# Kernel optimization log

Hardware: AMD Instinct MI355X
Metric: run time of the kernel (lower is better)

The kernel has to match this reference:

```python
import jax, jax.numpy as jnp
import numpy as np

N_NODES = 100000
N_EDGES = 1600000
D = 64
N_TARGETS = 100
N_GRAPHS = 512


def gcn_conv(x, W, b, src, dst):
    """GCNConv with default add_self_loops=True, symmetric normalization."""
    n = x.shape[0]
    h = x @ W  # [N, out]
    ones = jnp.ones(dst.shape[0], dtype=h.dtype)
    deg = jax.ops.segment_sum(ones, dst, num_segments=n) + 1.0  # +1 for self-loop
    dinv = jax.lax.rsqrt(deg)
    norm = dinv[src] * dinv[dst]  # [E]
    agg = jax.ops.segment_sum(h[src] * norm[:, None], dst, num_segments=n)
    agg = agg + h * (dinv * dinv)[:, None]  # self-loop contribution: 1/deg[i] * h[i]
    return agg + b


def setup_inputs() -> dict:
    key = jax.random.key(0)
    ks = jax.random.split(key, 12)
    x = jax.random.normal(ks[0], (N_NODES, D), dtype=jnp.float32)
    edge_index = jax.random.randint(ks[1], (2, N_EDGES), 0, N_NODES, dtype=jnp.int64)
    batch_seg = jnp.sort(jax.random.randint(ks[2], (N_NODES,), 0, N_GRAPHS, dtype=jnp.int64))
    s = 1.0 / np.sqrt(D)
    W1 = jax.random.normal(ks[3], (D, D), dtype=jnp.float32) * s
    b1 = jnp.zeros((D,), dtype=jnp.float32)
    W2 = jax.random.normal(ks[4], (D, D), dtype=jnp.float32) * s
    b2 = jnp.zeros((D,), dtype=jnp.float32)
    W3 = jax.random.normal(ks[5], (D, D), dtype=jnp.float32) * s
    b3 = jnp.zeros((D,), dtype=jnp.float32)
    Wout = jax.random.normal(ks[6], (D, N_TARGETS), dtype=jnp.float32) * s
    bout = jnp.zeros((N_TARGETS,), dtype=jnp.float32)
    return {"x": x, "W1": W1, "b1": b1, "W2": W2, "b2": b2, "W3": W3, "b3": b3,
            "Wout": Wout, "bout": bout, "edge_index": edge_index, "batch_seg": batch_seg}


def reference(x, W1, b1, W2, b2, W3, b3, Wout, bout, edge_index, batch_seg):
    src, dst = edge_index[0], edge_index[1]
    h = jax.nn.relu(gcn_conv(x, W1, b1, src, dst))   # dropout p=0 -> identity
    h = jax.nn.relu(gcn_conv(h, W2, b2, src, dst))
    h = gcn_conv(h, W3, b3, src, dst)
    counts = jax.ops.segment_sum(jnp.ones(h.shape[0], h.dtype), batch_seg, num_segments=N_GRAPHS)
    pooled = jax.ops.segment_sum(h, batch_seg, num_segments=N_GRAPHS) / jnp.maximum(counts, 1.0)[:, None]
    return pooled @ Wout + bout  # [N_GRAPHS, N_TARGETS]
```

## Files before the change

### kernel.cpp

```cpp
#include <hip/hip_runtime.h>

#define N_NODES   100000
#define N_EDGES   1600000
#define D         64
#define N_TARGETS 100
#define N_GRAPHS  512
#define NBUCK     391
#define EPB       4096
#define BCAP      6144
#define MM_NPW    16

typedef _Float16 half4 __attribute__((ext_vector_type(4)));
typedef _Float16 half8 __attribute__((ext_vector_type(8)));
typedef __fp16   hf2   __attribute__((ext_vector_type(2)));
typedef __fp16   hf8   __attribute__((ext_vector_type(8)));

#if defined(__has_builtin)
#if __has_builtin(__builtin_amdgcn_fdot2)
#define USE_DOT2 1
#endif
#endif

__global__ void k_init(int* __restrict__ gcur, float* __restrict__ poolz) {
    int i = blockIdx.x * blockDim.x + threadIdx.x;
    if (i < NBUCK) gcur[i] = 0;
    if (i < N_GRAPHS * D + N_GRAPHS) poolz[i] = 0.0f;
}

__global__ void k_prepW(const float* __restrict__ W, _Float16* __restrict__ out) {
    int t = threadIdx.x;
#pragma unroll
    for (int it = 0; it < 2; ++it) {
        int idx = t + it * 256;
        int m = idx >> 3, c = idx & 7;
        half8 hv;
#pragma unroll
        for (int tt = 0; tt < 8; ++tt)
            hv[tt] = (_Float16)W[(8 * c + tt) * 64 + m];
        *(half8*)&out[m * 64 + ((c ^ (m & 7)) * 8)] = hv;
    }
}

__global__ void __launch_bounds__(256)
k_binA(const int* __restrict__ src, const int* __restrict__ dst,
       int* __restrict__ gcur, unsigned long long* __restrict__ staged) {
    __shared__ int hist[NBUCK];
    __shared__ int boff[NBUCK];
    int tid = threadIdx.x;
    for (int i = tid; i < NBUCK; i += 256) hist[i] = 0;
    __syncthreads();

    int e0 = blockIdx.x * EPB;
    int s_[16], d_[16], r_[16];
#pragma unroll
    for (int k = 0; k < 16; ++k) {
        int e = e0 + k * 256 + tid;
        if (e < N_EDGES) {
            s_[k] = src[e];
            d_[k] = dst[e];
            r_[k] = atomicAdd(&hist[d_[k] >> 8], 1);
        } else {
            d_[k] = -1;
        }
    }
    __syncthreads();
    for (int b = tid; b < NBUCK; b += 256) {
        int h = hist[b];
        boff[b] = (h > 0) ? atomicAdd(&gcur[b], h) : 0;
    }
    __syncthreads();
#pragma unroll
    for (int k = 0; k < 16; ++k) {
        if (d_[k] >= 0) {
            int b = d_[k] >> 8;
            staged[(size_t)b * BCAP + boff[b] + r_[k]] =
                ((unsigned long long)(unsigned)d_[k] << 32) | (unsigned)s_[k];
        }
    }
}

__global__ void k_scanB(const int* __restrict__ gcur, int* __restrict__ bstart) {
    __shared__ int s[512];
    int t = threadIdx.x;
    int v = (t < NBUCK) ? gcur[t] : 0;
    s[t] = v;
    __syncthreads();
    for (int off = 1; off < 512; off <<= 1) {
        int x = (t >= off) ? s[t - off] : 0;
        __syncthreads();
        s[t] += x;
        __syncthreads();
    }
    if (t < NBUCK) bstart[t] = s[t] - v;
    if (t == 0) bstart[NBUCK] = N_EDGES;
}

__global__ void __launch_bounds__(256)
k_binB(const unsigned long long* __restrict__ staged, const int* __restrict__ gcur,
       const int* __restrict__ bstart, int* __restrict__ esrc,
       int* __restrict__ base, float* __restrict__ dinv) {
    __shared__ int s[256];
    __shared__ int lbase[256];
    __shared__ int cur[256];
    int b = blockIdx.x;
    int t = threadIdx.x;
    int n0 = b << 8;
    int Eb = gcur[b];
    int Sb = bstart[b];
    const unsigned long long* sl = staged + (size_t)b * BCAP;

    cur[t] = 0;
    __syncthreads();
    for (int k = t; k < Eb; k += 256) {
        int dl = ((int)(sl[k] >> 32)) & 255;
        atomicAdd(&cur[dl], 1);
    }
    __syncthreads();
    int v = cur[t];
    s[t] = v;
    __syncthreads();
    for (int off = 1; off < 256; off <<= 1) {
        int x = (t >= off) ? s[t - off] : 0;
        __syncthreads();
        s[t] += x;
        __syncthreads();
    }
    lbase[t] = s[t] - v;
    int gi = n0 + t;
    if (gi < N_NODES) {
        base[gi] = Sb + (s[t] - v);
        dinv[gi] = rsqrtf((float)v + 1.0f);
    }
    if (b == 0 && t == 0) base[N_NODES] = N_EDGES;
    cur[t] = 0;
    __syncthreads();
    for (int k = t; k < Eb; k += 256) {
        unsigned long long pd = sl[k];
        int dl = ((int)(pd >> 32)) & 255;
        int pos = Sb + lbase[dl] + atomicAdd(&cur[dl], 1);
        esrc[pos] = (int)(pd & 0xffffffffu);
    }
}

__global__ void __launch_bounds__(256)
k_mm(const float* __restrict__ X, const float* __restrict__ W,
     const float* __restrict__ dinv, _Float16* __restrict__ Y16) {
    __shared__ float W1L[D * D];
    __shared__ float aSh[4][D];
    int tid = threadIdx.x;
#pragma unroll
    for (int it = 0; it < 4; ++it) {
        int idx = (tid + it * 256) * 4;
        *(float4*)&W1L[idx] = *(const float4*)(W + idx);
    }
    __syncthreads();

    int wv = tid >> 6, lane = tid & 63;
    float wreg[D];
#pragma unroll
    for (int k = 0; k < D; ++k)
        wreg[k] = W1L[k * D + lane];

    int i0 = (blockIdx.x * 4 + wv) * MM_NPW;
    if (i0 >= N_NODES) return;
    int iEnd = i0 + MM_NPW; if (iEnd > N_NODES) iEnd = N_NODES;

    float xv = X[(size_t)i0 * D + lane];
    for (int i = i0; i < iEnd; ++i) {
        int inext = (i + 1 < N_NODES) ? (i + 1) : i;
        float xnext = X[(size_t)inext * D + lane];

        aSh[wv][lane] = xv;
        asm volatile("s_waitcnt lgkmcnt(0)" ::: "memory");

        float ac0 = 0.f, ac1 = 0.f, ac2 = 0.f, ac3 = 0.f;
#pragma unroll
        for (int c = 0; c < 16; ++c) {
            float4 a4 = *(const float4*)&aSh[wv][c * 4];
            ac0 = fmaf(a4.x, wreg[4 * c + 0], ac0);
            ac1 = fmaf(a4.y, wreg[4 * c + 1], ac1);
            ac2 = fmaf(a4.z, wreg[4 * c + 2], ac2);
            ac3 = fmaf(a4.w, wreg[4 * c + 3], ac3);
        }
        float acc = (ac0 + ac1) + (ac2 + ac3);
        Y16[(size_t)i * D + lane] = (_Float16)(acc * dinv[i]);
        xv = xnext;
    }
}

__global__ void __launch_bounds__(256)
k_pullmm(const _Float16* __restrict__ H, const int* __restrict__ esrc,
         const int* __restrict__ base, const float* __restrict__ dinv,
         const float* __restrict__ b_in, const _Float16* __restrict__ Whg,
         _Float16* __restrict__ Hout) {
    __shared__ _Float16 WhL[D * D];
    __shared__ _Float16 aSh[4][D];
    {
#pragma unroll
        for (int it = 0; it < 2; ++it) {
            int t = threadIdx.x + it * 256;
            *(half8*)&WhL[t * 8] = *(const half8*)&Whg[t * 8];
        }
    }
    __syncthreads();

    int wv   = threadIdx.x >> 6;
    int lane = threadIdx.x & 63;
    int g = lane >> 3, l = lane & 7;
    int i    = blockIdx.x * 4 + wv;
    int s0 = base[i], s1 = base[i + 1];

    float acc[8] = {0.f, 0.f, 0.f, 0.f, 0.f, 0.f, 0.f, 0.f};
    if (g == 0) {
        half8 sv = *(const half8*)(H + (size_t)i * D + l * 8);
#pragma unroll
        for (int q = 0; q < 8; ++q) acc[q] = (float)sv[q];
    }

    int p = s0;
    while (p < s1) {
        int cnt = s1 - p;
        if (cnt > 64) cnt = 64;
        int ed = (lane < cnt) ? esrc[p + lane] : 0;
        int j = 0;
        for (; j + 32 <= cnt; j += 32) {
            int e0 = __shfl(ed, j + g, 64);
            int e1 = __shfl(ed, j + 8 + g, 64);
            int e2 = __shfl(ed, j + 16 + g, 64);
            int e3 = __shfl(ed, j + 24 + g, 64);
            half8 v0 = *(const half8*)(H + (size_t)(unsigned)e0 * D + l * 8);
            half8 v1 = *(const half8*)(H + (size_t)(unsigned)e1 * D + l * 8);
            half8 v2 = *(const half8*)(H + (size_t)(unsigned)e2 * D + l * 8);
            half8 v3 = *(const half8*)(H + (size_t)(unsigned)e3 * D + l * 8);
            half8 s01 = v0 + v1;
            half8 s23 = v2 + v3;
#pragma unroll
            for (int q = 0; q < 8; ++q)
                acc[q] += (float)s01[q] + (float)s23[q];
        }
        for (; j + 8 <= cnt; j += 8) {
            int e0 = __shfl(ed, j + g, 64);
            half8 v0 = *(const half8*)(H + (size_t)(unsigned)e0 * D + l * 8);
#pragma unroll
            for (int q = 0; q < 8; ++q) acc[q] += (float)v0[q];
        }
        if (j < cnt) {
            int idx = j + g;
            int e0 = __shfl(ed, idx & 63, 64);
            if (idx < cnt) {
                half8 v0 = *(const half8*)(H + (size_t)(unsigned)e0 * D + l * 8);
#pragma unroll
                for (int q = 0; q < 8; ++q) acc[q] += (float)v0[q];
            }
        }
        p += cnt;
    }
#pragma unroll
    for (int off = 8; off <= 32; off <<= 1) {
#pragma unroll
        for (int q = 0; q < 8; ++q)
            acc[q] += __shfl_xor(acc[q], off, 64);
    }

    float di = dinv[i];
    if (g == 0) {
        float4 bl0 = *(const float4*)(b_in + l * 8);
        float4 bl1 = *(const float4*)(b_in + l * 8 + 4);
        half8 av;
        av[0] = (_Float16)fmaxf(fmaf(acc[0], di, bl0.x), 0.f);
        av[1] = (_Float16)fmaxf(fmaf(acc[1], di, bl0.y), 0.f);
        av[2] = (_Float16)fmaxf(fmaf(acc[2], di, bl0.z), 0.f);
        av[3] = (_Float16)fmaxf(fmaf(acc[3], di, bl0.w), 0.f);
        av[4] = (_Float16)fmaxf(fmaf(acc[4], di, bl1.x), 0.f);
        av[5] = (_Float16)fmaxf(fmaf(acc[5], di, bl1.y), 0.f);
        av[6] = (_Float16)fmaxf(fmaf(acc[6], di, bl1.z), 0.f);
        av[7] = (_Float16)fmaxf(fmaf(acc[7], di, bl1.w), 0.f);
        *(half8*)&aSh[wv][l * 8] = av;
    }
    asm volatile("s_waitcnt lgkmcnt(0)" ::: "memory");

    float part = 0.f;
#pragma unroll
    for (int c = 0; c < 8; ++c) {
        hf8 a8 = *(const hf8*)&aSh[wv][c * 8];
        hf8 w8 = *(const hf8*)&WhL[lane * 64 + ((c ^ (lane & 7)) * 8)];
#ifdef USE_DOT2
#pragma unroll
        for (int q = 0; q < 4; ++q) {
            hf2 ap; ap.x = a8[2 * q]; ap.y = a8[2 * q + 1];
            hf2 wp; wp.x = w8[2 * q]; wp.y = w8[2 * q + 1];
            part = __builtin_amdgcn_fdot2(ap, wp, part, false);
        }
#else
#pragma unroll
        for (int t = 0; t < 8; ++t)
            part = fmaf((float)a8[t], (float)w8[t], part);
#endif
    }
    Hout[(size_t)i * D + lane] = (_Float16)(part * di);
}

__global__ void __launch_bounds__(256)
k_pull(const _Float16* __restrict__ H, const int* __restrict__ esrc,
       const int* __restrict__ base, const float* __restrict__ dinv,
       const float* __restrict__ b, _Float16* __restrict__ AGG16) {
    int wv   = threadIdx.x >> 6;
    int lane = threadIdx.x & 63;
    int g = lane >> 3, l = lane & 7;
    int i    = blockIdx.x * 4 + wv;
    int s0 = base[i], s1 = base[i + 1];

    float acc[8] = {0.f, 0.f, 0.f, 0.f, 0.f, 0.f, 0.f, 0.f};
    if (g == 0) {
        half8 sv = *(const half8*)(H + (size_t)i * D + l * 8);
#pragma unroll
        for (int q = 0; q < 8; ++q) acc[q] = (float)sv[q];
    }

    int p = s0;
    while (p < s1) {
        int cnt = s1 - p;
        if (cnt > 64) cnt = 64;
        int ed = (lane < cnt) ? esrc[p + lane] : 0;
        int j = 0;
        for (; j + 32 <= cnt; j += 32) {
            int e0 = __shfl(ed, j + g, 64);
            int e1 = __shfl(ed, j + 8 + g, 64);
            int e2 = __shfl(ed, j + 16 + g, 64);
            int e3 = __shfl(ed, j + 24 + g, 64);
            half8 v0 = *(const half8*)(H + (size_t)(unsigned)e0 * D + l * 8);
            half8 v1 = *(const half8*)(H + (size_t)(unsigned)e1 * D + l * 8);
            half8 v2 = *(const half8*)(H + (size_t)(unsigned)e2 * D + l * 8);
            half8 v3 = *(const half8*)(H + (size_t)(unsigned)e3 * D + l * 8);
            half8 s01 = v0 + v1;
            half8 s23 = v2 + v3;
#pragma unroll
            for (int q = 0; q < 8; ++q)
                acc[q] += (float)s01[q] + (float)s23[q];
        }
        for (; j + 8 <= cnt; j += 8) {
            int e0 = __shfl(ed, j + g, 64);
            half8 v0 = *(const half8*)(H + (size_t)(unsigned)e0 * D + l * 8);
#pragma unroll
            for (int q = 0; q < 8; ++q) acc[q] += (float)v0[q];
        }
        if (j < cnt) {
            int idx = j + g;
            int e0 = __shfl(ed, idx & 63, 64);
            if (idx < cnt) {
                half8 v0 = *(const half8*)(H + (size_t)(unsigned)e0 * D + l * 8);
#pragma unroll
                for (int q = 0; q < 8; ++q) acc[q] += (float)v0[q];
            }
        }
        p += cnt;
    }
#pragma unroll
    for (int off = 8; off <= 32; off <<= 1) {
#pragma unroll
        for (int q = 0; q < 8; ++q)
            acc[q] += __shfl_xor(acc[q], off, 64);
    }

    if (g == 0) {
        float di = dinv[i];
        float4 bl0 = *(const float4*)(b + l * 8);
        float4 bl1 = *(const float4*)(b + l * 8 + 4);
        half8 o;
        o[0] = (_Float16)fmaf(acc[0], di, bl0.x);
        o[1] = (_Float16)fmaf(acc[1], di, bl0.y);
        o[2] = (_Float16)fmaf(acc[2], di, bl0.z);
        o[3] = (_Float16)fmaf(acc[3], di, bl0.w);
        o[4] = (_Float16)fmaf(acc[4], di, bl1.x);
        o[5] = (_Float16)fmaf(acc[5], di, bl1.y);
        o[6] = (_Float16)fmaf(acc[6], di, bl1.z);
        o[7] = (_Float16)fmaf(acc[7], di, bl1.w);
        *(half8*)(AGG16 + (size_t)i * D + l * 8) = o;
    }
}

__global__ void __launch_bounds__(256)
k_pool_seg(const _Float16* __restrict__ H16, const int* __restrict__ seg,
           float* __restrict__ pooled, float* __restrict__ counts) {
    int wave = threadIdx.x >> 6;
    int lane = threadIdx.x & 63;
    int n0 = (blockIdx.x * 4 + wave) * 64;
    if (n0 >= N_NODES) return;
    int nEnd = n0 + 64;
    if (nEnd > N_NODES) nEnd = N_NODES;
    int cur = seg[n0];
    float acc = 0.0f;
    int run = 0;
    for (int n = n0; n < nEnd; ++n) {
        int gsg = seg[n];
        if (gsg != cur) {
            atomicAdd(&pooled[(size_t)cur * D + lane], acc);
            if (lane == 0) atomicAdd(&counts[cur], (float)run);
            acc = 0.0f; run = 0;
            cur = gsg;
        }
        acc += (float)H16[(size_t)n * D + lane];
        run += 1;
    }
    atomicAdd(&pooled[(size_t)cur * D + lane], acc);
    if (lane == 0) atomicAdd(&counts[cur], (float)run);
}

__global__ void k_out(const float* __restrict__ pooled, const float* __restrict__ counts,
                      const float* __restrict__ Wout, const float* __restrict__ bout,
                      float* __restrict__ out) {
    __shared__ float prow[D];
    int g = blockIdx.x;
    int t = threadIdx.x;
    if (t < D) prow[t] = pooled[(size_t)g * D + t] / fmaxf(counts[g], 1.0f);
    __syncthreads();
    if (t < N_TARGETS) {
        float acc = bout[t];
#pragma unroll
        for (int k = 0; k < D; ++k)
            acc = fmaf(prow[k], Wout[k * N_TARGETS + t], acc);
        out[g * N_TARGETS + t] = acc;
    }
}


extern "C" void kernel_launch(void* const* d_in, const int* in_sizes, int n_in,
                              void* d_out, int out_size, void* d_ws, size_t ws_size,
                              hipStream_t stream) {
    const float* x    = (const float*)d_in[0];
    const float* W1   = (const float*)d_in[1];
    const float* b1   = (const float*)d_in[2];
    const float* W2   = (const float*)d_in[3];
    const float* b2   = (const float*)d_in[4];
    const float* W3   = (const float*)d_in[5];
    const float* b3   = (const float*)d_in[6];
    const float* Wout = (const float*)d_in[7];
    const float* bout = (const float*)d_in[8];
    const int*   eidx = (const int*)d_in[9];
    const int*   seg  = (const int*)d_in[10];
    const int* src = eidx;
    const int* dst = eidx + N_EDGES;
    float* out = (float*)d_out;

    _Float16* H16A   = (_Float16*)d_ws;
    _Float16* H16B   = H16A + (size_t)N_NODES * D;
    _Float16* AGG16  = H16B;
    unsigned long long* staged = (unsigned long long*)d_ws;
    int*      esrc   = (int*)(H16B + (size_t)N_NODES * D);
    float*    dinv   = (float*)(esrc + N_EDGES);
    int*      base   = (int*)(dinv + N_NODES);
    float*    pooled = (float*)(base + N_NODES + 4);
    float*    counts = pooled + N_GRAPHS * D;
    int*      gcur   = (int*)(counts + N_GRAPHS);
    int*      bstart = gcur + 512;
    _Float16* WhA    = (_Float16*)(bstart + 512);
    _Float16* WhB    = WhA + 4096;

    const int NB = (N_NODES + 255) / 256;

    k_prepW<<<1, 256, 0, stream>>>(W2, WhA);
    k_prepW<<<1, 256, 0, stream>>>(W3, WhB);

    k_init<<<130, 256, 0, stream>>>(gcur, pooled);
    k_binA<<<(N_EDGES + EPB - 1) / EPB, 256, 0, stream>>>(src, dst, gcur, staged);
    k_scanB<<<1, 512, 0, stream>>>(gcur, bstart);
    k_binB<<<NBUCK, 256, 0, stream>>>(staged, gcur, bstart, esrc, base, dinv);

    const int MMB = (N_NODES + 4 * MM_NPW - 1) / (4 * MM_NPW);
    k_mm<<<MMB, 256, 0, stream>>>(x, W1, dinv, H16A);
    k_pullmm<<<N_NODES / 4, 256, 0, stream>>>(H16A, esrc, base, dinv, b1, WhA, H16B);
    k_pullmm<<<N_NODES / 4, 256, 0, stream>>>(H16B, esrc, base, dinv, b2, WhB, H16A);
    k_pull<<<N_NODES / 4, 256, 0, stream>>>(H16A, esrc, base, dinv, b3, AGG16);

    k_pool_seg<<<NB, 256, 0, stream>>>(AGG16, seg, pooled, counts);
    k_out<<<N_GRAPHS, 128, 0, stream>>>(pooled, counts, Wout, bout, out);
}
```

Before: 347.1 us.

## Process multiple nodes per wave in pull kernels with LDS reduction

Each wave now handles four destination nodes in a loop, so the grid is four times smaller and the 8KB weight matrix loaded into LDS in k_pullmm is amortized over more nodes. The cross-group reduction of partial sums moves from a 24-shuffle butterfly to a store into shared memory followed by an 8-way read per lane. A 16-edge unrolled tail step is added to the gather loop. The trade-off is fewer waves in flight to hide gather latency and more load imbalance per wave, since nodes are processed serially.

```diff
diff --git a/kernel.cpp b/kernel.cpp
--- a/kernel.cpp
+++ b/kernel.cpp
@@ -9,6 +9,7 @@
 #define EPB       4096
 #define BCAP      6144
 #define MM_NPW    16
+#define NPN       4
 
 typedef _Float16 half4 __attribute__((ext_vector_type(4)));
 typedef _Float16 half8 __attribute__((ext_vector_type(8)));
@@ -194,6 +195,7 @@
          const float* __restrict__ b_in, const _Float16* __restrict__ Whg,
          _Float16* __restrict__ Hout) {
     __shared__ _Float16 WhL[D * D];
+    __shared__ float    red[4][8][D + 4];
     __shared__ _Float16 aSh[4][D];
     {
 #pragma unroll
@@ -207,175 +209,183 @@
     int wv   = threadIdx.x >> 6;
     int lane = threadIdx.x & 63;
     int g = lane >> 3, l = lane & 7;
-    int i    = blockIdx.x * 4 + wv;
-    int s0 = base[i], s1 = base[i + 1];
-
-    float acc[8] = {0.f, 0.f, 0.f, 0.f, 0.f, 0.f, 0.f, 0.f};
-    if (g == 0) {
-        half8 sv = *(const half8*)(H + (size_t)i * D + l * 8);
-#pragma unroll
-        for (int q = 0; q < 8; ++q) acc[q] = (float)sv[q];
-    }
-
-    int p = s0;
-    while (p < s1) {
-        int cnt = s1 - p;
-        if (cnt > 64) cnt = 64;
-        int ed = (lane < cnt) ? esrc[p + lane] : 0;
-        int j = 0;
-        for (; j + 32 <= cnt; j += 32) {
-            int e0 = __shfl(ed, j + g, 64);
-            int e1 = __shfl(ed, j + 8 + g, 64);
-            int e2 = __shfl(ed, j + 16 + g, 64);
-            int e3 = __shfl(ed, j + 24 + g, 64);
-            half8 v0 = *(const half8*)(H + (size_t)(unsigned)e0 * D + l * 8);
-            half8 v1 = *(const half8*)(H + (size_t)(unsigned)e1 * D + l * 8);
-            half8 v2 = *(const half8*)(H + (size_t)(unsigned)e2 * D + l * 8);
-            half8 v3 = *(const half8*)(H + (size_t)(unsigned)e3 * D + l * 8);
-            half8 s01 = v0 + v1;
-            half8 s23 = v2 + v3;
-#pragma unroll
-            for (int q = 0; q < 8; ++q)
-                acc[q] += (float)s01[q] + (float)s23[q];
-        }
-        for (; j + 8 <= cnt; j += 8) {
-            int e0 = __shfl(ed, j + g, 64);
-            half8 v0 = *(const half8*)(H + (size_t)(unsigned)e0 * D + l * 8);
-#pragma unroll
-            for (int q = 0; q < 8; ++q) acc[q] += (float)v0[q];
-        }
-        if (j < cnt) {
-            int idx = j + g;
-            int e0 = __shfl(ed, idx & 63, 64);
-            if (idx < cnt) {
+    float bias = b_in[lane];
+    int i0 = (blockIdx.x * 4 + wv) * NPN;
+
+    for (int n = 0; n < NPN; ++n) {
+        int i = i0 + n;
+        int s0 = base[i], s1 = base[i + 1];
+
+        float acc[8] = {0.f, 0.f, 0.f, 0.f, 0.f, 0.f, 0.f, 0.f};
+        if (g == 0) {
+            half8 sv = *(const half8*)(H + (size_t)i * D + l * 8);
+#pragma unroll
+            for (int q = 0; q < 8; ++q) acc[q] = (float)sv[q];
+        }
+
+        int p = s0;
+        while (p < s1) {
+            int cnt = s1 - p;
+            if (cnt > 64) cnt = 64;
+            int ed = (lane < cnt) ? esrc[p + lane] : 0;
+            int j = 0;
+            for (; j + 32 <= cnt; j += 32) {
+                int e0 = __shfl(ed, j + g, 64);
+                int e1 = __shfl(ed, j + 8 + g, 64);
+                int e2 = __shfl(ed, j + 16 + g, 64);
+                int e3 = __shfl(ed, j + 24 + g, 64);
+                half8 v0 = *(const half8*)(H + (size_t)(unsigned)e0 * D + l * 8);
+                half8 v1 = *(const half8*)(H + (size_t)(unsigned)e1 * D + l * 8);
+                half8 v2 = *(const half8*)(H + (size_t)(unsigned)e2 * D + l * 8);
+                half8 v3 = *(const half8*)(H + (size_t)(unsigned)e3 * D + l * 8);
+                half8 s01 = v0 + v1;
+                half8 s23 = v2 + v3;
+#pragma unroll
+                for (int q = 0; q < 8; ++q)
+                    acc[q] += (float)s01[q] + (float)s23[q];
+            }
+            for (; j + 16 <= cnt; j += 16) {
+                int e0 = __shfl(ed, j + g, 64);
+                int e1 = __shfl(ed, j + 8 + g, 64);
+                half8 v0 = *(const half8*)(H + (size_t)(unsigned)e0 * D + l * 8);
+                half8 v1 = *(const half8*)(H + (size_t)(unsigned)e1 * D + l * 8);
+                half8 s01 = v0 + v1;
+#pragma unroll
+                for (int q = 0; q < 8; ++q) acc[q] += (float)s01[q];
+            }
+            for (; j + 8 <= cnt; j += 8) {
+                int e0 = __shfl(ed, j + g, 64);
                 half8 v0 = *(const half8*)(H + (size_t)(unsigned)e0 * D + l * 8);
 #pragma unroll
                 for (int q = 0; q < 8; ++q) acc[q] += (float)v0[q];
             }
-        }
-        p += cnt;
-    }
-#pragma unroll
-    for (int off = 8; off <= 32; off <<= 1) {
-#pragma unroll
-        for (int q = 0; q < 8; ++q)
-            acc[q] += __shfl_xor(acc[q], off, 64);
-    }
-
-    float di = dinv[i];
-    if (g == 0) {
-        float4 bl0 = *(const float4*)(b_in + l * 8);
-        float4 bl1 = *(const float4*)(b_in + l * 8 + 4);
-        half8 av;
-        av[0] = (_Float16)fmaxf(fmaf(acc[0], di, bl0.x), 0.f);
-        av[1] = (_Float16)fmaxf(fmaf(acc[1], di, bl0.y), 0.f);
-        av[2] = (_Float16)fmaxf(fmaf(acc[2], di, bl0.z), 0.f);
-        av[3] = (_Float16)fmaxf(fmaf(acc[3], di, bl0.w), 0.f);
-        av[4] = (_Float16)fmaxf(fmaf(acc[4], di, bl1.x), 0.f);
-        av[5] = (_Float16)fmaxf(fmaf(acc[5], di, bl1.y), 0.f);
-        av[6] = (_Float16)fmaxf(fmaf(acc[6], di, bl1.z), 0.f);
-        av[7] = (_Float16)fmaxf(fmaf(acc[7], di, bl1.w), 0.f);
-        *(half8*)&aSh[wv][l * 8] = av;
-    }
-    asm volatile("s_waitcnt lgkmcnt(0)" ::: "memory");
-
-    float part = 0.f;
-#pragma unroll
-    for (int c = 0; c < 8; ++c) {
-        hf8 a8 = *(const hf8*)&aSh[wv][c * 8];
-        hf8 w8 = *(const hf8*)&WhL[lane * 64 + ((c ^ (lane & 7)) * 8)];
+            if (j < cnt) {
+                int idx = j + g;
+                int e0 = __shfl(ed, idx & 63, 64);
+                if (idx < cnt) {
+                    half8 v0 = *(const half8*)(H + (size_t)(unsigned)e0 * D + l * 8);
+#pragma unroll
+                    for (int q = 0; q < 8; ++q) acc[q] += (float)v0[q];
+                }
+            }
+            p += cnt;
+        }
+
+        *(float4*)&red[wv][g][l * 8]     = make_float4(acc[0], acc[1], acc[2], acc[3]);
+        *(float4*)&red[wv][g][l * 8 + 4] = make_float4(acc[4], acc[5], acc[6], acc[7]);
+        asm volatile("s_waitcnt lgkmcnt(0)" ::: "memory");
+        float agg = 0.f;
+#pragma unroll
+        for (int gg = 0; gg < 8; ++gg)
+            agg += red[wv][gg][lane];
+
+        float di = dinv[i];
+        float av = fmaxf(fmaf(agg, di, bias), 0.f);
+        aSh[wv][lane] = (_Float16)av;
+        asm volatile("s_waitcnt lgkmcnt(0)" ::: "memory");
+
+        float part = 0.f;
+#pragma unroll
+        for (int c = 0; c < 8; ++c) {
+            hf8 a8 = *(const hf8*)&aSh[wv][c * 8];
+            hf8 w8 = *(const hf8*)&WhL[lane * 64 + ((c ^ (lane & 7)) * 8)];
 #ifdef USE_DOT2
 #pragma unroll
-        for (int q = 0; q < 4; ++q) {
-            hf2 ap; ap.x = a8[2 * q]; ap.y = a8[2 * q + 1];
-            hf2 wp; wp.x = w8[2 * q]; wp.y = w8[2 * q + 1];
-            part = __builtin_amdgcn_fdot2(ap, wp, part, false);
-        }
+            for (int q = 0; q < 4; ++q) {
+                hf2 ap; ap.x = a8[2 * q]; ap.y = a8[2 * q + 1];
+                hf2 wp; wp.x = w8[2 * q]; wp.y = w8[2 * q + 1];
+                part = __builtin_amdgcn_fdot2(ap, wp, part, false);
+            }
 #else
 #pragma unroll
-        for (int t = 0; t < 8; ++t)
-            part = fmaf((float)a8[t], (float)w8[t], part);
+            for (int t = 0; t < 8; ++t)
+                part = fmaf((float)a8[t], (float)w8[t], part);
 #endif
-    }
-    Hout[(size_t)i * D + lane] = (_Float16)(part * di);
+        }
+        Hout[(size_t)i * D + lane] = (_Float16)(part * di);
+    }
 }
 
 __global__ void __launch_bounds__(256)
 k_pull(const _Float16* __restrict__ H, const int* __restrict__ esrc,
        const int* __restrict__ base, const float* __restrict__ dinv,
        const float* __restrict__ b, _Float16* __restrict__ AGG16) {
+    __shared__ float red[4][8][D + 4];
     int wv   = threadIdx.x >> 6;
     int lane = threadIdx.x & 63;
     int g = lane >> 3, l = lane & 7;
-    int i    = blockIdx.x * 4 + wv;
-    int s0 = base[i], s1 = base[i + 1];
-
-    float acc[8] = {0.f, 0.f, 0.f, 0.f, 0.f, 0.f, 0.f, 0.f};
-    if (g == 0) {
-        half8 sv = *(const half8*)(H + (size_t)i * D + l * 8);
-#pragma unroll
-        for (int q = 0; q < 8; ++q) acc[q] = (float)sv[q];
-    }
-
-    int p = s0;
-    while (p < s1) {
-        int cnt = s1 - p;
-        if (cnt > 64) cnt = 64;
-        int ed = (lane < cnt) ? esrc[p + lane] : 0;
-        int j = 0;
-        for (; j + 32 <= cnt; j += 32) {
-            int e0 = __shfl(ed, j + g, 64);
-            int e1 = __shfl(ed, j + 8 + g, 64);
-            int e2 = __shfl(ed, j + 16 + g, 64);
-            int e3 = __shfl(ed, j + 24 + g, 64);
-            half8 v0 = *(const half8*)(H + (size_t)(unsigned)e0 * D + l * 8);
-            half8 v1 = *(const half8*)(H + (size_t)(unsigned)e1 * D + l * 8);
-            half8 v2 = *(const half8*)(H + (size_t)(unsigned)e2 * D + l * 8);
-            half8 v3 = *(const half8*)(H + (size_t)(unsigned)e3 * D + l * 8);
-            half8 s01 = v0 + v1;
-            half8 s23 = v2 + v3;
-#pragma unroll
-            for (int q = 0; q < 8; ++q)
-                acc[q] += (float)s01[q] + (float)s23[q];
-        }
-        for (; j + 8 <= cnt; j += 8) {
-            int e0 = __shfl(ed, j + g, 64);
-            half8 v0 = *(const half8*)(H + (size_t)(unsigned)e0 * D + l * 8);
-#pragma unroll
-            for (int q = 0; q < 8; ++q) acc[q] += (float)v0[q];
-        }
-        if (j < cnt) {
-            int idx = j + g;
-            int e0 = __shfl(ed, idx & 63, 64);
-            if (idx < cnt) {
+    float bias = b[lane];
+    int i0 = (blockIdx.x * 4 + wv) * NPN;
+
+    for (int n = 0; n < NPN; ++n) {
+        int i = i0 + n;
+        int s0 = base[i], s1 = base[i + 1];
+
+        float acc[8] = {0.f, 0.f, 0.f, 0.f, 0.f, 0.f, 0.f, 0.f};
+        if (g == 0) {
+            half8 sv = *(const half8*)(H + (size_t)i * D + l * 8);
+#pragma unroll
+            for (int q = 0; q < 8; ++q) acc[q] = (float)sv[q];
+        }
+
+        int p = s0;
+        while (p < s1) {
+            int cnt = s1 - p;
+            if (cnt > 64) cnt = 64;
+            int ed = (lane < cnt) ? esrc[p + lane] : 0;
+            int j = 0;
+            for (; j + 32 <= cnt; j += 32) {
+                int e0 = __shfl(ed, j + g, 64);
+                int e1 = __shfl(ed, j + 8 + g, 64);
+                int e2 = __shfl(ed, j + 16 + g, 64);
+                int e3 = __shfl(ed, j + 24 + g, 64);
+                half8 v0 = *(const half8*)(H + (size_t)(unsigned)e0 * D + l * 8);
+                half8 v1 = *(const half8*)(H + (size_t)(unsigned)e1 * D + l * 8);
+                half8 v2 = *(const half8*)(H + (size_t)(unsigned)e2 * D + l * 8);
+                half8 v3 = *(const half8*)(H + (size_t)(unsigned)e3 * D + l * 8);
+                half8 s01 = v0 + v1;
+                half8 s23 = v2 + v3;
+#pragma unroll
+                for (int q = 0; q < 8; ++q)
+                    acc[q] += (float)s01[q] + (float)s23[q];
+            }
+            for (; j + 16 <= cnt; j += 16) {
+                int e0 = __shfl(ed, j + g, 64);
+                int e1 = __shfl(ed, j + 8 + g, 64);
+                half8 v0 = *(const half8*)(H + (size_t)(unsigned)e0 * D + l * 8);
+                half8 v1 = *(const half8*)(H + (size_t)(unsigned)e1 * D + l * 8);
+                half8 s01 = v0 + v1;
+#pragma unroll
+                for (int q = 0; q < 8; ++q) acc[q] += (float)s01[q];
+            }
+            for (; j + 8 <= cnt; j += 8) {
+                int e0 = __shfl(ed, j + g, 64);
                 half8 v0 = *(const half8*)(H + (size_t)(unsigned)e0 * D + l * 8);
 #pragma unroll
                 for (int q = 0; q < 8; ++q) acc[q] += (float)v0[q];
             }
-        }
-        p += cnt;
-    }
-#pragma unroll
-    for (int off = 8; off <= 32; off <<= 1) {
-#pragma unroll
-        for (int q = 0; q < 8; ++q)
-            acc[q] += __shfl_xor(acc[q], off, 64);
-    }
-
-    if (g == 0) {
-        float di = dinv[i];
-        float4 bl0 = *(const float4*)(b + l * 8);
-        float4 bl1 = *(const float4*)(b + l * 8 + 4);
-        half8 o;
-        o[0] = (_Float16)fmaf(acc[0], di, bl0.x);
-        o[1] = (_Float16)fmaf(acc[1], di, bl0.y);
-        o[2] = (_Float16)fmaf(acc[2], di, bl0.z);
-        o[3] = (_Float16)fmaf(acc[3], di, bl0.w);
-        o[4] = (_Float16)fmaf(acc[4], di, bl1.x);
-        o[5] = (_Float16)fmaf(acc[5], di, bl1.y);
-        o[6] = (_Float16)fmaf(acc[6], di, bl1.z);
-        o[7] = (_Float16)fmaf(acc[7], di, bl1.w);
-        *(half8*)(AGG16 + (size_t)i * D + l * 8) = o;
+            if (j < cnt) {
+                int idx = j + g;
+                int e0 = __shfl(ed, idx & 63, 64);
+                if (idx < cnt) {
+                    half8 v0 = *(const half8*)(H + (size_t)(unsigned)e0 * D + l * 8);
+#pragma unroll
+                    for (int q = 0; q < 8; ++q) acc[q] += (float)v0[q];
+                }
+            }
+            p += cnt;
+        }
+
+        *(float4*)&red[wv][g][l * 8]     = make_float4(acc[0], acc[1], acc[2], acc[3]);
+        *(float4*)&red[wv][g][l * 8 + 4] = make_float4(acc[4], acc[5], acc[6], acc[7]);
+        asm volatile("s_waitcnt lgkmcnt(0)" ::: "memory");
+        float agg = 0.f;
+#pragma unroll
+        for (int gg = 0; gg < 8; ++gg)
+            agg += red[wv][gg][lane];
+        asm volatile("s_waitcnt lgkmcnt(0)" ::: "memory");
+
+        AGG16[(size_t)i * D + lane] = (_Float16)fmaf(agg, dinv[i], bias);
     }
 }
 
@@ -467,10 +477,11 @@
     k_binB<<<NBUCK, 256, 0, stream>>>(staged, gcur, bstart, esrc, base, dinv);
 
     const int MMB = (N_NODES + 4 * MM_NPW - 1) / (4 * MM_NPW);
+    const int PB  = N_NODES / (4 * NPN);
     k_mm<<<MMB, 256, 0, stream>>>(x, W1, dinv, H16A);
-    k_pullmm<<<N_NODES / 4, 256, 0, stream>>>(H16A, esrc, base, dinv, b1, WhA, H16B);
-    k_pullmm<<<N_NODES / 4, 256, 0, stream>>>(H16B, esrc, base, dinv, b2, WhB, H16A);
-    k_pull<<<N_NODES / 4, 256, 0, stream>>>(H16A, esrc, base, dinv, b3, AGG16);
+    k_pullmm<<<PB, 256, 0, stream>>>(H16A, esrc, base, dinv, b1, WhA, H16B);
+    k_pullmm<<<PB, 256, 0, stream>>>(H16B, esrc, base, dinv, b2, WhB, H16A);
+    k_pull<<<PB, 256, 0, stream>>>(H16A, esrc, base, dinv, b3, AGG16);
 
     k_pool_seg<<<NB, 256, 0, stream>>>(AGG16, seg, pooled, counts);
     k_out<<<N_GRAPHS, 128, 0, stream>>>(pooled, counts, Wout, bout, out);
```

New measurement: 320.2 us. 7.8% less time.
